# Kernel tuning notes

Hardware: AMD Instinct MI355X
Metric: run time of the kernel (lower is better)

Reference implementation:

```python
import jax, jax.numpy as jnp
import numpy as np
import math

V, D, H, KVH, L, T, B = 32000, 1024, 16, 4, 4, 2048, 2
HD = D // H            # head_dim = 64
GROUP = H // KVH       # GQA group size = 4
KVW = KVH * HD         # kv width = 256
EPS = 1e-5


def _alibi_slopes(n_heads):
    # n_heads=16 is a power of two
    start = 2.0 ** (-2.0 ** (-(math.log2(n_heads) - 3)))
    return np.array([start * start ** i for i in range(n_heads)], dtype=np.float32)


def setup_inputs() -> dict:
    key = jax.random.key(0)
    ks = jax.random.split(key, 8)
    s = 0.02
    inp = {
        "tok_emb": jax.random.normal(ks[0], (V, D), jnp.float32) * s,
        "ln1_s": jnp.ones((L, D), jnp.float32),
        "ln1_b": jnp.zeros((L, D), jnp.float32),
        "qkv_w": jax.random.normal(ks[1], (L, D, D + 2 * KVW), jnp.float32) * s,
        "qkv_b": jnp.zeros((L, D + 2 * KVW), jnp.float32),
        "proj_w": jax.random.normal(ks[2], (L, D, D), jnp.float32) * s,
        "proj_b": jnp.zeros((L, D), jnp.float32),
        "ln2_s": jnp.ones((L, D), jnp.float32),
        "ln2_b": jnp.zeros((L, D), jnp.float32),
        "fc1_w": jax.random.normal(ks[3], (L, D, 4 * D), jnp.float32) * s,
        "fc1_b": jnp.zeros((L, 4 * D), jnp.float32),
        "fc2_w": jax.random.normal(ks[4], (L, 4 * D, D), jnp.float32) * s,
        "fc2_b": jnp.zeros((L, D), jnp.float32),
        "lnf_s": jnp.ones((D,), jnp.float32),
        "lnf_b": jnp.zeros((D,), jnp.float32),
        "idx": jax.random.randint(ks[5], (B, T), 0, V, jnp.int32),
    }
    return inp


def _ln(x, s, b):
    mu = jnp.mean(x, axis=-1, keepdims=True)
    var = jnp.var(x, axis=-1, keepdims=True)
    return (x - mu) * jax.lax.rsqrt(var + EPS) * s + b


def _forward(tok_emb, ln1_s, ln1_b, qkv_w, qkv_b, proj_w, proj_b,
             ln2_s, ln2_b, fc1_w, fc1_b, fc2_w, fc2_b, lnf_s, lnf_b, idx):
    x = tok_emb[idx]  # (B, T, D); ALiBi => no learned positional embedding

    # combined causal mask + ALiBi bias: (1, H, T, T)
    slopes = jnp.asarray(_alibi_slopes(H)).reshape(1, H, 1, 1)
    pos = jnp.arange(T, dtype=jnp.float32)
    rel = jnp.minimum(pos[None, :] - pos[:, None], 0.0)  # (T, T), clamp_max(0)
    causal = pos[None, :] <= pos[:, None]
    bias = jnp.where(causal[None, None], rel[None, None] * slopes, -jnp.inf)

    scale = 1.0 / math.sqrt(HD)
    for l in range(L):
        h = _ln(x, ln1_s[l], ln1_b[l])
        qkv = h @ qkv_w[l] + qkv_b[l]
        q = qkv[..., :D].reshape(B, T, H, HD).transpose(0, 2, 1, 3)
        k = qkv[..., D:D + KVW].reshape(B, T, KVH, HD).transpose(0, 2, 1, 3)
        v = qkv[..., D + KVW:].reshape(B, T, KVH, HD).transpose(0, 2, 1, 3)
        k = jnp.repeat(k, GROUP, axis=1)  # GQA broadcast -> (B, H, T, HD)
        v = jnp.repeat(v, GROUP, axis=1)
        att = jnp.einsum("bhqd,bhkd->bhqk", q, k) * scale + bias
        att = jax.nn.softmax(att, axis=-1)
        o = jnp.einsum("bhqk,bhkd->bhqd", att, v)
        o = o.transpose(0, 2, 1, 3).reshape(B, T, D)
        x = x + o @ proj_w[l] + proj_b[l]
        h = _ln(x, ln2_s[l], ln2_b[l])
        x = x + jax.nn.gelu(h @ fc1_w[l] + fc1_b[l], approximate=False) @ fc2_w[l] + fc2_b[l]

    x = _ln(x, lnf_s, lnf_b)
    logits = x @ tok_emb.T  # tied head (no bias)
    return logits


def reference(tok_emb, ln1_s, ln1_b, qkv_w, qkv_b, proj_w, proj_b,
              ln2_s, ln2_b, fc1_w, fc1_b, fc2_w, fc2_b, lnf_s, lnf_b, idx):
    return _forward(tok_emb, ln1_s, ln1_b, qkv_w, qkv_b, proj_w, proj_b,
                    ln2_s, ln2_b, fc1_w, fc1_b, fc2_w, fc2_b, lnf_s, lnf_b, idx)
```

## Files before the change

### kernel.cpp

```cpp
#include <hip/hip_runtime.h>

#define DEV __device__ __forceinline__
typedef unsigned short u16;
typedef __bf16 bf16_t;
typedef bf16_t bf16x8 __attribute__((ext_vector_type(8)));
typedef float f32x4 __attribute__((ext_vector_type(4)));

DEV u16 f2bf(float f){ unsigned u=__float_as_uint(f); return (u16)((u + 0x7fffu + ((u>>16)&1u))>>16); }

DEV void gl_lds16(const void* g, void* l){
  __builtin_amdgcn_global_load_lds((__attribute__((address_space(1))) void*)g,
                                   (__attribute__((address_space(3))) void*)l, 16, 0, 0);
}
DEV f32x4 MFMA(bf16x8 a, bf16x8 b, f32x4 c){
  return __builtin_amdgcn_mfma_f32_16x16x32_bf16(a, b, c, 0, 0, 0);
}
DEV bf16x8 ld8(const u16* p){ return *(const bf16x8*)p; }

__global__ __launch_bounds__(256) void k_prep(const float* __restrict__ emb,
                                              u16* __restrict__ te,
                                              const int* __restrict__ idx,
                                              float* __restrict__ x){
  int b = blockIdx.x;
  if(b < 32000){
    int i = b*256 + threadIdx.x;
    float4 v = ((const float4*)emb)[i];
    ushort4 o; o.x=f2bf(v.x); o.y=f2bf(v.y); o.z=f2bf(v.z); o.w=f2bf(v.w);
    ((ushort4*)te)[i] = o;
  } else {
    int row = b - 32000;
    int tok = idx[row];
    ((float4*)(x + (size_t)row*1024))[threadIdx.x] =
        ((const float4*)(emb + (size_t)tok*1024))[threadIdx.x];
  }
}

__global__ __launch_bounds__(256) void k_ln(const float* __restrict__ x,
                                            const float* __restrict__ sc,
                                            const float* __restrict__ bi,
                                            u16* __restrict__ out){
  int row = blockIdx.x;
  const float* xr = x + (size_t)row*1024;
  float4 v = ((const float4*)xr)[threadIdx.x];
  float s = v.x+v.y+v.z+v.w;
  float q = v.x*v.x+v.y*v.y+v.z*v.z+v.w*v.w;
  #pragma unroll
  for(int m=1;m<64;m<<=1){ s += __shfl_xor(s,m); q += __shfl_xor(q,m); }
  __shared__ float ss[4], sq[4];
  int w = threadIdx.x>>6;
  if((threadIdx.x&63)==0){ ss[w]=s; sq[w]=q; }
  __syncthreads();
  s = ss[0]+ss[1]+ss[2]+ss[3];
  q = sq[0]+sq[1]+sq[2]+sq[3];
  float mu = s*(1.f/1024.f);
  float var = q*(1.f/1024.f) - mu*mu;
  float rs = rsqrtf(var + 1e-5f);
  float4 sv = ((const float4*)sc)[threadIdx.x];
  float4 bv = ((const float4*)bi)[threadIdx.x];
  ushort4 o;
  o.x = f2bf((v.x-mu)*rs*sv.x + bv.x);
  o.y = f2bf((v.y-mu)*rs*sv.y + bv.y);
  o.z = f2bf((v.z-mu)*rs*sv.z + bv.z);
  o.w = f2bf((v.w-mu)*rs*sv.w + bv.w);
  *(ushort4*)(out + (size_t)row*1024 + threadIdx.x*4) = o;
}

__global__ __launch_bounds__(256) void k_convT(const float* __restrict__ W,
                                               u16* __restrict__ Wt, int K, int N){
  __shared__ float tile[64][68];
  size_t loff = (size_t)blockIdx.z * K * N;
  W  += loff;  Wt += loff;
  int n0 = blockIdx.x*64, k0 = blockIdx.y*64;
  int tx = threadIdx.x & 15, ty = threadIdx.x >> 4;
  #pragma unroll
  for(int r=0;r<4;r++){
    int row = ty + r*16;
    float4 v = *(const float4*)&W[(size_t)(k0+row)*N + n0 + tx*4];
    *(float4*)&tile[row][tx*4] = v;
  }
  __syncthreads();
  int nn = threadIdx.x >> 2, kq = threadIdx.x & 3;
  #pragma unroll
  for(int r=0;r<4;r++){
    int k = (kq + r*4)*4;
    ushort4 o;
    o.x = f2bf(tile[k+0][nn]); o.y = f2bf(tile[k+1][nn]);
    o.z = f2bf(tile[k+2][nn]); o.w = f2bf(tile[k+3][nn]);
    *(ushort4*)&Wt[(size_t)(n0+nn)*K + k0 + k] = o;
  }
}

template<int EPI, int SWAP>
__global__ __launch_bounds__(256) void k_gemm(const u16* __restrict__ A,
                                              const u16* __restrict__ Bt,
                                              const float* __restrict__ bias,
                                              void* __restrict__ out,
                                              float* __restrict__ res,
                                              int M, int N, int K, int m_base){
  __shared__ __align__(16) u16 As[128*64];
  __shared__ __align__(16) u16 Bs[128*64];
  int t = threadIdx.x, l = t & 63, w = t >> 6;
  int g = l >> 4, lr = l & 15;
  int wr = w >> 1, wc = w & 1;
  int m0, n0;
  if constexpr(SWAP){ m0 = m_base + blockIdx.x*128; n0 = blockIdx.y*128; }
  else              { m0 = m_base + blockIdx.y*128; n0 = blockIdx.x*128; }
  f32x4 acc[4][4];
  #pragma unroll
  for(int i=0;i<4;i++)
    #pragma unroll
    for(int j=0;j<4;j++) acc[i][j] = f32x4{0.f,0.f,0.f,0.f};

  int sr = t >> 3;
  int sc = (((t & 7) ^ (sr & 7)) * 8);
  const u16* pa = A  + (size_t)(m0 + sr)*K + sc;
  const u16* pb = Bt + (size_t)(n0 + sr)*K + sc;
  u16* lda = As + t*8;
  u16* ldb = Bs + t*8;
  const int rs_a = (lr & 7)*8;

  for(int k0=0; k0<K; k0+=64){
    #pragma unroll
    for(int i=0;i<4;i++){
      gl_lds16(pa + (size_t)(i*32)*K, lda + i*2048);
      gl_lds16(pb + (size_t)(i*32)*K, ldb + i*2048);
    }
    pa += 64; pb += 64;
    __syncthreads();
    bf16x8 af[4][2], bfr[4][2];
    #pragma unroll
    for(int mi=0;mi<4;mi++){
      int row = wr*64 + mi*16 + lr;
      af[mi][0] = ld8(&As[row*64 + ((g*8     ) ^ rs_a)]);
      af[mi][1] = ld8(&As[row*64 + ((g*8 + 32) ^ rs_a)]);
    }
    #pragma unroll
    for(int ni=0;ni<4;ni++){
      int row = wc*64 + ni*16 + lr;
      bfr[ni][0] = ld8(&Bs[row*64 + ((g*8     ) ^ rs_a)]);
      bfr[ni][1] = ld8(&Bs[row*64 + ((g*8 + 32) ^ rs_a)]);
    }
    #pragma unroll
    for(int mi=0;mi<4;mi++)
      #pragma unroll
      for(int ni=0;ni<4;ni++){
        acc[mi][ni] = MFMA(af[mi][0], bfr[ni][0], acc[mi][ni]);
        acc[mi][ni] = MFMA(af[mi][1], bfr[ni][1], acc[mi][ni]);
      }
    __syncthreads();
  }

  float bv[4];
  #pragma unroll
  for(int ni=0;ni<4;ni++){
    if constexpr(EPI==3) bv[ni] = 0.f;
    else bv[ni] = bias[n0 + wc*64 + ni*16 + lr];
  }
  #pragma unroll
  for(int mi=0;mi<4;mi++){
    int row = m0 + wr*64 + mi*16 + g*4;
    #pragma unroll
    for(int ni=0;ni<4;ni++){
      int col = n0 + wc*64 + ni*16 + lr;
      #pragma unroll
      for(int r=0;r<4;r++){
        float v = acc[mi][ni][r] + bv[ni];
        size_t oidx = (size_t)(row + r)*N + col;
        if constexpr(EPI==0){
          ((u16*)out)[oidx] = f2bf(v);
        } else if constexpr(EPI==1){
          res[oidx] += v;
        } else if constexpr(EPI==2){
          float gv = 0.5f*v*(1.f + erff(v*0.70710678118654752f));
          ((u16*)out)[oidx] = f2bf(gv);
        } else {
          ((float*)out)[oidx] = v;
        }
      }
    }
  }
}

template<int EPI>
__global__ __launch_bounds__(256) void k_gemm_n64(const u16* __restrict__ A,
                                                  const u16* __restrict__ Bt,
                                                  const float* __restrict__ bias,
                                                  void* __restrict__ outp,
                                                  float* __restrict__ res,
                                                  int M, int N, int K){
  __shared__ __align__(16) u16 As[128*64];
  __shared__ __align__(16) u16 Bs[64*64];
  int t = threadIdx.x, l = t & 63, w = t >> 6;
  int g = l >> 4, lr = l & 15;
  int wr = w >> 1, wc = w & 1;
  int m0 = blockIdx.y*128, n0 = blockIdx.x*64;
  f32x4 acc[4][2];
  #pragma unroll
  for(int i=0;i<4;i++)
    #pragma unroll
    for(int j=0;j<2;j++) acc[i][j] = f32x4{0.f,0.f,0.f,0.f};

  int sr = t >> 3;
  int sc = (((t & 7) ^ (sr & 7)) * 8);
  const u16* pa = A  + (size_t)(m0 + sr)*K + sc;
  const u16* pb = Bt + (size_t)(n0 + sr)*K + sc;
  u16* lda = As + t*8;
  u16* ldb = Bs + t*8;
  const int rs_a = (lr & 7)*8;

  for(int k0=0; k0<K; k0+=64){
    #pragma unroll
    for(int i=0;i<4;i++)
      gl_lds16(pa + (size_t)(i*32)*K, lda + i*2048);
    #pragma unroll
    for(int i=0;i<2;i++)
      gl_lds16(pb + (size_t)(i*32)*K, ldb + i*2048);
    pa += 64; pb += 64;
    __syncthreads();
    bf16x8 af[4][2], bfr[2][2];
    #pragma unroll
    for(int mi=0;mi<4;mi++){
      int row = wr*64 + mi*16 + lr;
      af[mi][0] = ld8(&As[row*64 + ((g*8     ) ^ rs_a)]);
      af[mi][1] = ld8(&As[row*64 + ((g*8 + 32) ^ rs_a)]);
    }
    #pragma unroll
    for(int ni=0;ni<2;ni++){
      int row = wc*32 + ni*16 + lr;
      bfr[ni][0] = ld8(&Bs[row*64 + ((g*8     ) ^ rs_a)]);
      bfr[ni][1] = ld8(&Bs[row*64 + ((g*8 + 32) ^ rs_a)]);
    }
    #pragma unroll
    for(int mi=0;mi<4;mi++)
      #pragma unroll
      for(int ni=0;ni<2;ni++){
        acc[mi][ni] = MFMA(af[mi][0], bfr[ni][0], acc[mi][ni]);
        acc[mi][ni] = MFMA(af[mi][1], bfr[ni][1], acc[mi][ni]);
      }
    __syncthreads();
  }

  float bv[2];
  #pragma unroll
  for(int ni=0;ni<2;ni++) bv[ni] = bias[n0 + wc*32 + ni*16 + lr];
  #pragma unroll
  for(int mi=0;mi<4;mi++){
    int row = m0 + wr*64 + mi*16 + g*4;
    #pragma unroll
    for(int ni=0;ni<2;ni++){
      int col = n0 + wc*32 + ni*16 + lr;
      #pragma unroll
      for(int r=0;r<4;r++){
        float v = acc[mi][ni][r] + bv[ni];
        if constexpr(EPI==0)
          ((u16*)outp)[(size_t)(row + r)*N + col] = f2bf(v);
        else
          res[(size_t)(row + r)*N + col] += v;
      }
    }
  }
}

__global__ __launch_bounds__(512) void k_gemm256(const u16* __restrict__ A,
                                                 const u16* __restrict__ Bt,
                                                 float* __restrict__ out,
                                                 int M, int N, int K, int m_base){
  __shared__ __align__(16) u16 As[2][256*64];
  __shared__ __align__(16) u16 Bs[2][256*64];
  int t = threadIdx.x, l = t & 63, wid = t >> 6;
  int g = l >> 4, lr = l & 15;
  int m0 = m_base + blockIdx.x*256, n0 = blockIdx.y*256;
  f32x4 acc[2][16];
  #pragma unroll
  for(int mi=0;mi<2;mi++)
    #pragma unroll
    for(int i=0;i<16;i++) acc[mi][i] = f32x4{0.f,0.f,0.f,0.f};

  int srow = t >> 3;
  int scol = ((t & 7) ^ (srow & 7)) * 8;
  const int rs = (lr & 7) * 8;
  int nt = K >> 6;

  auto stage_half = [&](int jj, int h){
    int buf = jj & 1; int k0s = jj << 6;
    if(h < 2){
      #pragma unroll
      for(int c=0;c<2;c++){
        int rr = h*128 + c*64 + srow;
        gl_lds16(A + (size_t)(m0 + rr)*K + k0s + scol,
                 &As[buf][rr*64 + (t&7)*8]);
      }
    } else {
      #pragma unroll
      for(int c=0;c<2;c++){
        int rr = (h-2)*128 + c*64 + srow;
        gl_lds16(Bt + (size_t)(n0 + rr)*K + k0s + scol,
                 &Bs[buf][rr*64 + (t&7)*8]);
      }
    }
  };

  stage_half(0,0); stage_half(0,1); stage_half(0,2); stage_half(0,3);
  asm volatile("s_waitcnt vmcnt(2)" ::: "memory");
  __builtin_amdgcn_s_barrier();
  __builtin_amdgcn_sched_barrier(0);

  bf16x8 af[2][2];
  for(int j=0; j<nt; ++j){
    const u16* Ab = As[j & 1];
    const u16* Bb = Bs[j & 1];
    bool pf = (j + 1 < nt);
    #pragma unroll
    for(int q=0; q<4; ++q){
      if(q == 0){
        #pragma unroll
        for(int mi=0;mi<2;mi++){
          int row = wid*32 + mi*16 + lr;
          af[mi][0] = ld8(&Ab[row*64 + ((g*8     ) ^ rs)]);
          af[mi][1] = ld8(&Ab[row*64 + ((g*8 + 32) ^ rs)]);
        }
      }
      bf16x8 bfr[4][2];
      #pragma unroll
      for(int i=0;i<4;i++){
        int row = (q*4 + i)*16 + lr;
        bfr[i][0] = ld8(&Bb[row*64 + ((g*8     ) ^ rs)]);
        bfr[i][1] = ld8(&Bb[row*64 + ((g*8 + 32) ^ rs)]);
      }
      if(pf) stage_half(j+1, q);
      __builtin_amdgcn_s_barrier();
      __builtin_amdgcn_sched_barrier(0);
      __builtin_amdgcn_s_setprio(1);
      #pragma unroll
      for(int mi=0;mi<2;mi++)
        #pragma unroll
        for(int i=0;i<4;i++){
          acc[mi][q*4+i] = MFMA(af[mi][0], bfr[i][0], acc[mi][q*4+i]);
          acc[mi][q*4+i] = MFMA(af[mi][1], bfr[i][1], acc[mi][q*4+i]);
        }
      __builtin_amdgcn_s_setprio(0);
      if(q == 1) asm volatile("s_waitcnt vmcnt(4)" ::: "memory");
      if(q == 3) asm volatile("s_waitcnt vmcnt(2)" ::: "memory");
      __builtin_amdgcn_s_barrier();
      __builtin_amdgcn_sched_barrier(0);
    }
  }

  #pragma unroll
  for(int mi=0;mi<2;mi++){
    int row = m0 + wid*32 + mi*16 + g*4;
    #pragma unroll
    for(int i=0;i<16;i++){
      int col = n0 + i*16 + lr;
      #pragma unroll
      for(int r=0;r<4;r++)
        out[(size_t)(row + r)*N + col] = acc[mi][i][r];
    }
  }
}

__global__ __launch_bounds__(256) void k_gemm_f32b(const u16* __restrict__ A,
                                                   const float* __restrict__ B,
                                                   float* __restrict__ out,
                                                   int M, int N, int K, int m_base){
  __shared__ __align__(16) u16 As[128*32];
  __shared__ __align__(16) u16 Bs[128*32];
  int t = threadIdx.x, l = t & 63, w = t >> 6;
  int g = l >> 4, lr = l & 15;
  int wr = w >> 1, wc = w & 1;
  int m0 = m_base + blockIdx.y*128, n0 = blockIdx.x*128;
  f32x4 acc[4][4];
  #pragma unroll
  for(int i=0;i<4;i++)
    #pragma unroll
    for(int j=0;j<4;j++) acc[i][j] = f32x4{0.f,0.f,0.f,0.f};

  int r0 = t >> 2, c0 = (t & 3)*8;
  const u16* pa0 = A + (size_t)(m0 + r0)*K + c0;
  const u16* pa1 = A + (size_t)(m0 + r0 + 64)*K + c0;
  u16* la0 = As + t*8;  u16* la1 = As + (t+256)*8;
  int br = t >> 1, bc = (t & 1)*16;
  const float* pb = B + (size_t)(n0 + br)*K + bc;

  for(int k0=0; k0<K; k0+=32){
    gl_lds16(pa0, la0); gl_lds16(pa1, la1);
    pa0 += 32; pa1 += 32;
    float4 f0 = ((const float4*)pb)[0];
    float4 f1 = ((const float4*)pb)[1];
    float4 f2 = ((const float4*)pb)[2];
    float4 f3 = ((const float4*)pb)[3];
    pb += 32;
    ushort4 u0{f2bf(f0.x),f2bf(f0.y),f2bf(f0.z),f2bf(f0.w)};
    ushort4 u1{f2bf(f1.x),f2bf(f1.y),f2bf(f1.z),f2bf(f1.w)};
    ushort4 u2{f2bf(f2.x),f2bf(f2.y),f2bf(f2.z),f2bf(f2.w)};
    ushort4 u3{f2bf(f3.x),f2bf(f3.y),f2bf(f3.z),f2bf(f3.w)};
    *(ushort4*)&Bs[br*32 + bc +  0] = u0;
    *(ushort4*)&Bs[br*32 + bc +  4] = u1;
    *(ushort4*)&Bs[br*32 + bc +  8] = u2;
    *(ushort4*)&Bs[br*32 + bc + 12] = u3;
    __syncthreads();
    bf16x8 af[4], bfr[4];
    #pragma unroll
    for(int mi=0;mi<4;mi++) af[mi]  = ld8(&As[(wr*64 + mi*16 + lr)*32 + g*8]);
    #pragma unroll
    for(int ni=0;ni<4;ni++) bfr[ni] = ld8(&Bs[(wc*64 + ni*16 + lr)*32 + g*8]);
    #pragma unroll
    for(int mi=0;mi<4;mi++)
      #pragma unroll
      for(int ni=0;ni<4;ni++)
        acc[mi][ni] = MFMA(af[mi], bfr[ni], acc[mi][ni]);
    __syncthreads();
  }

  #pragma unroll
  for(int mi=0;mi<4;mi++){
    int row = m0 + wr*64 + mi*16 + g*4;
    #pragma unroll
    for(int ni=0;ni<4;ni++){
      int col = n0 + wc*64 + ni*16 + lr;
      #pragma unroll
      for(int r=0;r<4;r++)
        out[(size_t)(row + r)*N + col] = acc[mi][ni][r];
    }
  }
}

__global__ __launch_bounds__(512) void k_attn(const u16* __restrict__ qkv,
                                              u16* __restrict__ atto){
  __shared__ __align__(16) u16 Ksm[64*72];
  __shared__ __align__(16) u16 Vsm[64*72];
  __shared__ __align__(16) u16 Psm[8][16*72];
  int t = threadIdx.x, l = t & 63, w = t >> 6, g = l >> 4, lr = l & 15;
  int bh = blockIdx.y; int b = bh >> 4, h = bh & 15, kvh = h >> 2;
  int qb = blockIdx.x * 128;
  const float L2E = 1.44269504088896f;
  const float C1  = 0.125f * L2E;
  float slopeL = exp2f(-0.5f*(float)(h+1)) * L2E;
  float sLkt[4];
  #pragma unroll
  for(int kt=0;kt<4;kt++) sLkt[kt] = slopeL*(float)(kt*16+lr);

  int qrow = qb + w*16 + lr;
  const u16* qp = qkv + (size_t)(b*2048 + qrow)*1536 + h*64;
  bf16x8 qf0 = ld8(qp + g*8);
  bf16x8 qf1 = ld8(qp + 32 + g*8);

  bf16_t onev = (bf16_t)1.0f;
  bf16x8 onesb = {onev,onev,onev,onev,onev,onev,onev,onev};

  f32x4 oacc[4];
  #pragma unroll
  for(int i=0;i<4;i++) oacc[i] = f32x4{0.f,0.f,0.f,0.f};
  f32x4 lsum = f32x4{0.f,0.f,0.f,0.f};

  int qmin_w = qb + w*16;
  int qmax_w = qmin_w + 15;
  int nkb = blockIdx.x*2 + 2;
  for(int kb=0; kb<nkb; kb++){
    __syncthreads();
    {
      int key = t >> 3, ho = (t & 7)*8;
      const u16* src = qkv + (size_t)(b*2048 + kb*64 + key)*1536 + 1024 + kvh*64 + ho;
      *(int4*)&Ksm[key*72 + ho] = *(const int4*)src;
    }
    if(t < 256){
      int key0 = (t>>3)*2, hd0 = (t&7)*8;
      const u16* v0 = qkv + (size_t)(b*2048 + kb*64 + key0)*1536 + 1280 + kvh*64 + hd0;
      int4 A0 = *(const int4*)v0;
      int4 A1 = *(const int4*)(v0 + 1536);
      const u16* ua = (const u16*)&A0; const u16* ub = (const u16*)&A1;
      #pragma unroll
      for(int j=0;j<8;j++){
        int row = hd0 + j;
        int colp = key0 ^ ((row>>3)*8);
        unsigned pr = (unsigned)ua[j] | ((unsigned)ub[j]<<16);
        *(unsigned*)&Vsm[row*72 + colp] = pr;
      }
    }
    __syncthreads();
    if(kb*64 > qmax_w) continue;
    f32x4 sacc[4];
    #pragma unroll
    for(int kt=0;kt<4;kt++) sacc[kt] = f32x4{0.f,0.f,0.f,0.f};
    #pragma unroll
    for(int kt=0;kt<4;kt++){
      bf16x8 kf0 = ld8(&Ksm[(kt*16+lr)*72 + g*8]);
      bf16x8 kf1 = ld8(&Ksm[(kt*16+lr)*72 + 32 + g*8]);
      sacc[kt] = MFMA(qf0, kf0, sacc[kt]);
      sacc[kt] = MFMA(qf1, kf1, sacc[kt]);
    }
    if(kb*64 + 63 <= qmin_w){
      #pragma unroll
      for(int r=0;r<4;r++){
        int q = qb + w*16 + g*4 + r;
        float base = slopeL*(float)(kb*64 - q) - 8.0f*L2E;
        #pragma unroll
        for(int kt=0;kt<4;kt++){
          float f = fmaf(sacc[kt][r], C1, base + sLkt[kt]);
          Psm[w][(g*4+r)*72 + kt*16 + lr] = f2bf(exp2f(f));
        }
      }
    } else {
      #pragma unroll
      for(int r=0;r<4;r++){
        int q = qb + w*16 + g*4 + r;
        float base = slopeL*(float)(kb*64 - q) - 8.0f*L2E;
        #pragma unroll
        for(int kt=0;kt<4;kt++){
          int key = kb*64 + kt*16 + lr;
          float f = fmaf(sacc[kt][r], C1, base + sLkt[kt]);
          float p = (key <= q) ? exp2f(f) : 0.f;
          Psm[w][(g*4+r)*72 + kt*16 + lr] = f2bf(p);
        }
      }
    }
    #pragma unroll
    for(int ks=0;ks<2;ks++){
      bf16x8 pf = ld8(&Psm[w][lr*72 + ks*32 + g*8]);
      lsum = MFMA(pf, onesb, lsum);
      #pragma unroll
      for(int ht=0;ht<4;ht++){
        int row = ht*16 + lr;
        int colp = (ks*32 + g*8) ^ ((row>>3)*8);
        bf16x8 vf = ld8(&Vsm[row*72 + colp]);
        oacc[ht] = MFMA(pf, vf, oacc[ht]);
      }
    }
  }
  #pragma unroll
  for(int ht=0;ht<4;ht++){
    #pragma unroll
    for(int r=0;r<4;r++){
      float o = oacc[ht][r] / lsum[r];
      atto[(size_t)(b*2048 + qb + w*16 + g*4 + r)*1024 + h*64 + ht*16 + lr] = f2bf(o);
    }
  }
}

extern "C" void kernel_launch(void* const* d_in, const int* in_sizes, int n_in,
                              void* d_out, int out_size, void* d_ws, size_t ws_size,
                              hipStream_t stream) {
  const float* tok_emb = (const float*)d_in[0];
  const float* ln1_s   = (const float*)d_in[1];
  const float* ln1_b   = (const float*)d_in[2];
  const float* qkv_w   = (const float*)d_in[3];
  const float* qkv_b   = (const float*)d_in[4];
  const float* proj_w  = (const float*)d_in[5];
  const float* proj_b  = (const float*)d_in[6];
  const float* ln2_s   = (const float*)d_in[7];
  const float* ln2_b   = (const float*)d_in[8];
  const float* fc1_w   = (const float*)d_in[9];
  const float* fc1_b   = (const float*)d_in[10];
  const float* fc2_w   = (const float*)d_in[11];
  const float* fc2_b   = (const float*)d_in[12];
  const float* lnf_s   = (const float*)d_in[13];
  const float* lnf_b   = (const float*)d_in[14];
  const int*   idx     = (const int*)d_in[15];

  char* ob = (char*)d_out;
  float* xf32  = (float*)(ob);
  u16* qkv_bf  = (u16*)(ob + (size_t)16777216);
  u16* atto_bf = (u16*)(ob + (size_t)29360128);
  u16* mid_bf  = (u16*)(ob + (size_t)37748736);
  u16* wt_qkv  = (u16*)(ob + (size_t)71303168);
  u16* wt_proj = (u16*)(ob + (size_t)83886080);
  u16* wt_fc1  = (u16*)(ob + (size_t)92274688);
  u16* wt_fc2  = (u16*)(ob + (size_t)125829120);
  u16* h_bf    = (u16*)d_ws;
  float* out   = (float*)d_out;

  bool big_ws = ws_size >= (size_t)(8388608 + 65536000);
  u16* te_bf = big_ws ? (u16*)((char*)d_ws + 8388608)
                      : (u16*)(ob + (size_t)294912000);

  k_prep<<<36096, 256, 0, stream>>>(tok_emb, te_bf, idx, xf32);
  k_convT<<<dim3(24,16,4), 256, 0, stream>>>(qkv_w,  wt_qkv, 1024, 1536);
  k_convT<<<dim3(16,16,4), 256, 0, stream>>>(proj_w, wt_proj, 1024, 1024);
  k_convT<<<dim3(64,16,4), 256, 0, stream>>>(fc1_w, wt_fc1, 1024, 4096);
  k_convT<<<dim3(16,64,4), 256, 0, stream>>>(fc2_w, wt_fc2, 4096, 1024);

  for(int l=0; l<4; l++){
    k_ln<<<4096, 256, 0, stream>>>(xf32, ln1_s + (size_t)l*1024, ln1_b + (size_t)l*1024, h_bf);
    k_gemm_n64<0><<<dim3(24,32), 256, 0, stream>>>(h_bf, wt_qkv + (size_t)l*1536*1024,
                                                   qkv_b + (size_t)l*1536,
                                                   qkv_bf, nullptr, 4096, 1536, 1024);
    k_attn<<<dim3(16,32), 512, 0, stream>>>(qkv_bf, atto_bf);
    k_gemm_n64<1><<<dim3(16,32), 256, 0, stream>>>(atto_bf, wt_proj + (size_t)l*1024*1024,
                                                   proj_b + (size_t)l*1024,
                                                   nullptr, xf32, 4096, 1024, 1024);
    k_ln<<<4096, 256, 0, stream>>>(xf32, ln2_s + (size_t)l*1024, ln2_b + (size_t)l*1024, h_bf);
    k_gemm<2,0><<<dim3(32,32), 256, 0, stream>>>(h_bf, wt_fc1 + (size_t)l*4096*1024,
                                                 fc1_b + (size_t)l*4096,
                                                 mid_bf, nullptr, 4096, 4096, 1024, 0);
    k_gemm_n64<1><<<dim3(16,32), 256, 0, stream>>>(mid_bf, wt_fc2 + (size_t)l*1024*4096,
                                                   fc2_b + (size_t)l*1024,
                                                   nullptr, xf32, 4096, 1024, 4096);
  }
  k_ln<<<4096, 256, 0, stream>>>(xf32, lnf_s, lnf_b, h_bf);

  if(big_ws){
    k_gemm256<<<dim3(16,125), 512, 0, stream>>>(h_bf, te_bf, out,
                                                4096, 32000, 1024, 0);
  } else {
    k_gemm256<<<dim3(9,125), 512, 0, stream>>>(h_bf, te_bf, out,
                                               4096, 32000, 1024, 0);
    k_gemm256<<<dim3(5,125), 512, 0, stream>>>(h_bf, te_bf, out,
                                               4096, 32000, 1024, 2816);
    k_gemm_f32b<<<dim3(250,4), 256, 0, stream>>>(h_bf, tok_emb, out,
                                                 4096, 32000, 1024, 2304);
  }
}
```

Baseline: 1.554 ms.

## Process two 16-row query tiles per wave in attention, halving block threads

The attention kernel now runs 4 waves of 256 threads instead of 8 waves, and each wave handles 32 query rows as two 16-row MFMA tiles. Each K and V fragment read from LDS feeds two MFMAs. This halves LDS fragment traffic per query and the number of waves sharing each K/V tile load. The cost is more registers per wave (double accumulators) and fewer waves for hiding latency. Causal skipping is also coarser, at 32-row granularity per wave.

```diff
diff --git a/kernel.cpp b/kernel.cpp
--- a/kernel.cpp
+++ b/kernel.cpp
@@ -425,11 +425,11 @@
   }
 }
 
-__global__ __launch_bounds__(512) void k_attn(const u16* __restrict__ qkv,
+__global__ __launch_bounds__(256) void k_attn(const u16* __restrict__ qkv,
                                               u16* __restrict__ atto){
   __shared__ __align__(16) u16 Ksm[64*72];
   __shared__ __align__(16) u16 Vsm[64*72];
-  __shared__ __align__(16) u16 Psm[8][16*72];
+  __shared__ __align__(16) u16 Psm[4][32*72];
   int t = threadIdx.x, l = t & 63, w = t >> 6, g = l >> 4, lr = l & 15;
   int bh = blockIdx.y; int b = bh >> 4, h = bh & 15, kvh = h >> 2;
   int qb = blockIdx.x * 128;
@@ -440,30 +440,32 @@
   #pragma unroll
   for(int kt=0;kt<4;kt++) sLkt[kt] = slopeL*(float)(kt*16+lr);
 
-  int qrow = qb + w*16 + lr;
-  const u16* qp = qkv + (size_t)(b*2048 + qrow)*1536 + h*64;
-  bf16x8 qf0 = ld8(qp + g*8);
-  bf16x8 qf1 = ld8(qp + 32 + g*8);
+  const u16* qp0 = qkv + (size_t)(b*2048 + qb + w*32 + lr)*1536 + h*64;
+  const u16* qp1 = qp0 + (size_t)16*1536;
+  bf16x8 qA0 = ld8(qp0 + g*8),  qA1 = ld8(qp0 + 32 + g*8);
+  bf16x8 qB0 = ld8(qp1 + g*8),  qB1 = ld8(qp1 + 32 + g*8);
 
   bf16_t onev = (bf16_t)1.0f;
   bf16x8 onesb = {onev,onev,onev,onev,onev,onev,onev,onev};
 
-  f32x4 oacc[4];
-  #pragma unroll
-  for(int i=0;i<4;i++) oacc[i] = f32x4{0.f,0.f,0.f,0.f};
-  f32x4 lsum = f32x4{0.f,0.f,0.f,0.f};
-
-  int qmin_w = qb + w*16;
-  int qmax_w = qmin_w + 15;
+  f32x4 oaccA[4], oaccB[4];
+  #pragma unroll
+  for(int i=0;i<4;i++){ oaccA[i] = f32x4{0.f,0.f,0.f,0.f}; oaccB[i] = f32x4{0.f,0.f,0.f,0.f}; }
+  f32x4 lsumA = f32x4{0.f,0.f,0.f,0.f}, lsumB = f32x4{0.f,0.f,0.f,0.f};
+
+  int qmin_w = qb + w*32;
+  int qmax_w = qmin_w + 31;
   int nkb = blockIdx.x*2 + 2;
   for(int kb=0; kb<nkb; kb++){
     __syncthreads();
-    {
-      int key = t >> 3, ho = (t & 7)*8;
+    #pragma unroll
+    for(int i=0;i<2;i++){
+      int tt = t + i*256;
+      int key = tt >> 3, ho = (tt & 7)*8;
       const u16* src = qkv + (size_t)(b*2048 + kb*64 + key)*1536 + 1024 + kvh*64 + ho;
       *(int4*)&Ksm[key*72 + ho] = *(const int4*)src;
     }
-    if(t < 256){
+    {
       int key0 = (t>>3)*2, hd0 = (t&7)*8;
       const u16* v0 = qkv + (size_t)(b*2048 + kb*64 + key0)*1536 + 1280 + kvh*64 + hd0;
       int4 A0 = *(const int4*)v0;
@@ -479,51 +481,62 @@
     }
     __syncthreads();
     if(kb*64 > qmax_w) continue;
-    f32x4 sacc[4];
-    #pragma unroll
-    for(int kt=0;kt<4;kt++) sacc[kt] = f32x4{0.f,0.f,0.f,0.f};
+    f32x4 sA[4], sB[4];
+    #pragma unroll
+    for(int kt=0;kt<4;kt++){ sA[kt] = f32x4{0.f,0.f,0.f,0.f}; sB[kt] = f32x4{0.f,0.f,0.f,0.f}; }
     #pragma unroll
     for(int kt=0;kt<4;kt++){
       bf16x8 kf0 = ld8(&Ksm[(kt*16+lr)*72 + g*8]);
       bf16x8 kf1 = ld8(&Ksm[(kt*16+lr)*72 + 32 + g*8]);
-      sacc[kt] = MFMA(qf0, kf0, sacc[kt]);
-      sacc[kt] = MFMA(qf1, kf1, sacc[kt]);
+      sA[kt] = MFMA(qA0, kf0, sA[kt]);  sA[kt] = MFMA(qA1, kf1, sA[kt]);
+      sB[kt] = MFMA(qB0, kf0, sB[kt]);  sB[kt] = MFMA(qB1, kf1, sB[kt]);
     }
     if(kb*64 + 63 <= qmin_w){
       #pragma unroll
       for(int r=0;r<4;r++){
-        int q = qb + w*16 + g*4 + r;
-        float base = slopeL*(float)(kb*64 - q) - 8.0f*L2E;
+        int qA = qb + w*32 + g*4 + r;
+        float baseA = slopeL*(float)(kb*64 - qA) - 8.0f*L2E;
+        float baseB = baseA - slopeL*16.0f;
         #pragma unroll
         for(int kt=0;kt<4;kt++){
-          float f = fmaf(sacc[kt][r], C1, base + sLkt[kt]);
-          Psm[w][(g*4+r)*72 + kt*16 + lr] = f2bf(exp2f(f));
+          float fA = fmaf(sA[kt][r], C1, baseA + sLkt[kt]);
+          float fB = fmaf(sB[kt][r], C1, baseB + sLkt[kt]);
+          Psm[w][(g*4+r)*72 + kt*16 + lr]      = f2bf(exp2f(fA));
+          Psm[w][(16 + g*4+r)*72 + kt*16 + lr] = f2bf(exp2f(fB));
         }
       }
     } else {
       #pragma unroll
       for(int r=0;r<4;r++){
-        int q = qb + w*16 + g*4 + r;
-        float base = slopeL*(float)(kb*64 - q) - 8.0f*L2E;
+        int qA = qb + w*32 + g*4 + r;
+        int qB = qA + 16;
+        float baseA = slopeL*(float)(kb*64 - qA) - 8.0f*L2E;
+        float baseB = baseA - slopeL*16.0f;
         #pragma unroll
         for(int kt=0;kt<4;kt++){
           int key = kb*64 + kt*16 + lr;
-          float f = fmaf(sacc[kt][r], C1, base + sLkt[kt]);
-          float p = (key <= q) ? exp2f(f) : 0.f;
-          Psm[w][(g*4+r)*72 + kt*16 + lr] = f2bf(p);
+          float fA = fmaf(sA[kt][r], C1, baseA + sLkt[kt]);
+          float fB = fmaf(sB[kt][r], C1, baseB + sLkt[kt]);
+          float pA = (key <= qA) ? exp2f(fA) : 0.f;
+          float pB = (key <= qB) ? exp2f(fB) : 0.f;
+          Psm[w][(g*4+r)*72 + kt*16 + lr]      = f2bf(pA);
+          Psm[w][(16 + g*4+r)*72 + kt*16 + lr] = f2bf(pB);
         }
       }
     }
     #pragma unroll
     for(int ks=0;ks<2;ks++){
-      bf16x8 pf = ld8(&Psm[w][lr*72 + ks*32 + g*8]);
-      lsum = MFMA(pf, onesb, lsum);
+      bf16x8 pfA = ld8(&Psm[w][lr*72 + ks*32 + g*8]);
+      bf16x8 pfB = ld8(&Psm[w][(16+lr)*72 + ks*32 + g*8]);
+      lsumA = MFMA(pfA, onesb, lsumA);
+      lsumB = MFMA(pfB, onesb, lsumB);
       #pragma unroll
       for(int ht=0;ht<4;ht++){
         int row = ht*16 + lr;
         int colp = (ks*32 + g*8) ^ ((row>>3)*8);
         bf16x8 vf = ld8(&Vsm[row*72 + colp]);
-        oacc[ht] = MFMA(pf, vf, oacc[ht]);
+        oaccA[ht] = MFMA(pfA, vf, oaccA[ht]);
+        oaccB[ht] = MFMA(pfB, vf, oaccB[ht]);
       }
     }
   }
@@ -531,8 +544,9 @@
   for(int ht=0;ht<4;ht++){
     #pragma unroll
     for(int r=0;r<4;r++){
-      float o = oacc[ht][r] / lsum[r];
-      atto[(size_t)(b*2048 + qb + w*16 + g*4 + r)*1024 + h*64 + ht*16 + lr] = f2bf(o);
+      size_t rowA = (size_t)(b*2048 + qb + w*32 + g*4 + r);
+      atto[rowA*1024 + h*64 + ht*16 + lr]        = f2bf(oaccA[ht][r] / lsumA[r]);
+      atto[(rowA+16)*1024 + h*64 + ht*16 + lr]   = f2bf(oaccB[ht][r] / lsumB[r]);
     }
   }
 }
@@ -584,7 +598,7 @@
     k_gemm_n64<0><<<dim3(24,32), 256, 0, stream>>>(h_bf, wt_qkv + (size_t)l*1536*1024,
                                                    qkv_b + (size_t)l*1536,
                                                    qkv_bf, nullptr, 4096, 1536, 1024);
-    k_attn<<<dim3(16,32), 512, 0, stream>>>(qkv_bf, atto_bf);
+    k_attn<<<dim3(16,32), 256, 0, stream>>>(qkv_bf, atto_bf);
     k_gemm_n64<1><<<dim3(16,32), 256, 0, stream>>>(atto_bf, wt_proj + (size_t)l*1024*1024,
                                                    proj_b + (size_t)l*1024,
                                                    nullptr, xf32, 4096, 1024, 1024);
```

Result: no change. 1.571 ms (+1.1%).
